# Performance work log

Hardware: AMD Instinct MI355X
Metric: run time of the kernel (lower is better)

## Reference

```python
import jax, jax.numpy as jnp
import numpy as np

B, T, D, DFF = 8, 2048, 1024, 4096
EPS = 1e-6
PLIF_ALPHA = 2.0


@jax.custom_vjp
def spike_fn(m):
    # hard threshold forward, atan surrogate backward (PLIF neuron)
    return (m > 0.0).astype(m.dtype)

def _spk_fwd(m):
    return (m > 0.0).astype(m.dtype), m

def _spk_bwd(m, g):
    ds = PLIF_ALPHA / (2.0 * (1.0 + (jnp.pi * 0.5 * PLIF_ALPHA * m) ** 2))
    return (g * ds,)

spike_fn.defvjp(_spk_fwd, _spk_bwd)


def _rmsnorm(x, w):
    rstd = jax.lax.rsqrt(jnp.mean(x * x, axis=-1, keepdims=True) + EPS)
    return x * rstd * w


def setup_inputs() -> dict:
    key = jax.random.key(0)
    ks = jax.random.split(key, 9)
    sc = 0.02
    return {
        'x': jax.random.normal(ks[0], (B, T, D), jnp.float32),
        'rms_w1': jnp.ones((D,), jnp.float32),
        'rms_w2': jnp.ones((D,), jnp.float32),
        'delta_w': sc * jax.random.normal(ks[1], (D, D), jnp.float32),
        'delta_b': jnp.zeros((D,), jnp.float32),
        'b_w': sc * jax.random.normal(ks[2], (D, D), jnp.float32),
        'b_b': jnp.zeros((D,), jnp.float32),
        'A_log': jnp.log(jnp.linspace(0.5, 2.0, D).astype(jnp.float32)),
        'log_tau': jnp.full((D,), jnp.log(2.0), jnp.float32),
        'plif_thr': jnp.ones((D,), jnp.float32),
        'syn_w': sc * jax.random.normal(ks[3], (D, D), jnp.float32),
        'syn_b': jnp.zeros((D,), jnp.float32),
        'gate_w': sc * jax.random.normal(ks[4], (D, D), jnp.float32),
        'gate_b': jnp.zeros((D,), jnp.float32),
        'ffn_g_w': sc * jax.random.normal(ks[5], (DFF, D), jnp.float32),
        'ffn_u_w': sc * jax.random.normal(ks[6], (DFF, D), jnp.float32),
        'ffn_d_w': sc * jax.random.normal(ks[7], (D, DFF), jnp.float32),
    }


def _forward(x, rms_w1, rms_w2, delta_w, delta_b, b_w, b_b, A_log, log_tau,
             plif_thr, syn_w, syn_b, gate_w, gate_b, ffn_g_w, ffn_u_w, ffn_d_w):
    Bx, Tx, Dx = x.shape
    # --- RMSNorm 1 ---
    y1 = _rmsnorm(x, rms_w1)
    # --- selective-scan style liquid inputs ---
    delta = jax.nn.softplus(jnp.einsum('btd,ed->bte', y1, delta_w) + delta_b)  # [B,T,D]
    bvec = delta * (jnp.einsum('btd,ed->bte', y1, b_w) + b_b)                  # [B,T,D]
    A = jnp.exp(-delta * jnp.exp(A_log))                                        # [B,T,D]

    # --- liquid recurrent scan: h_t = tanh(A_t * h_{t-1} + b_t) ---
    def liquid_step(h, ab):
        a_t, b_t = ab
        h = jnp.tanh(a_t * h + b_t)
        return h, h

    h0 = jnp.zeros((Bx, Dx), x.dtype)
    _, h_post = jax.lax.scan(liquid_step, h0,
                             (jnp.swapaxes(A, 0, 1), jnp.swapaxes(bvec, 0, 1)))
    h_post = jnp.swapaxes(h_post, 0, 1)  # [B,T,D]

    # --- PLIF spiking scan with soft reset ---
    pdec = jnp.exp(-1.0 / jnp.exp(log_tau))  # [D]

    def plif_step(v, h_t):
        v_pre = pdec * v + (1.0 - pdec) * h_t
        s = spike_fn(v_pre - plif_thr)
        return v_pre - s * plif_thr, s

    v0 = jnp.zeros((Bx, Dx), x.dtype)
    _, spike = jax.lax.scan(plif_step, v0, jnp.swapaxes(h_post, 0, 1))
    spike = jnp.swapaxes(spike, 0, 1)

    # --- SEW shortcut + synaptic gate ---
    spike_in = spike + h_post
    syn = jnp.einsum('btd,ed->bte', spike_in, syn_w) + syn_b
    gate = jax.nn.sigmoid(jnp.einsum('btd,ed->bte', spike_in, gate_w) + gate_b)
    x1 = x + syn * gate

    # --- RMSNorm 2 + SwiGLU FFN + residual ---
    y2 = _rmsnorm(x1, rms_w2)
    ffn_act = jax.nn.silu(y2 @ ffn_g_w.T) * (y2 @ ffn_u_w.T)
    return x1 + ffn_act @ ffn_d_w.T


def reference(x, rms_w1, rms_w2, delta_w, delta_b, b_w, b_b, A_log, log_tau,
              plif_thr, syn_w, syn_b, gate_w, gate_b, ffn_g_w, ffn_u_w, ffn_d_w):
    return _forward(x, rms_w1, rms_w2, delta_w, delta_b, b_w, b_b, A_log,
                    log_tau, plif_thr, syn_w, syn_b, gate_w, gate_b,
                    ffn_g_w, ffn_u_w, ffn_d_w)
```

## Files before the change

### kernel.cpp

```cpp
#include <hip/hip_runtime.h>
#include <stdint.h>

#define B_   8
#define T_   2048
#define D_   1024
#define DFF_ 4096
#define M_   (B_ * T_)

typedef __bf16 bf16;
typedef bf16  bf16x8 __attribute__((ext_vector_type(8)));
typedef bf16  bf16x4 __attribute__((ext_vector_type(4)));
typedef float f32x4  __attribute__((ext_vector_type(4)));

#define CAST_LDS(p) ((__attribute__((address_space(3))) void*)(p))
#define CAST_GLB(p) ((const __attribute__((address_space(1))) void*)(p))

struct CvtArgs {
    const float* s[7];
    bf16* d[7];
    int nblk[7];
};

__global__ __launch_bounds__(256) void f2bf_all_kernel(CvtArgs a) {
    int blk = blockIdx.x;
    int seg = 0;
#pragma unroll
    for (int i = 0; i < 7; ++i) seg += (blk >= a.nblk[i]) ? 1 : 0;
    const int base = (seg == 0) ? 0 : a.nblk[seg - 1];
    const int i = ((blk - base) * 256 + threadIdx.x) * 4;
    const float4 v = *(const float4*)(a.s[seg] + i);
    bf16x4 o;
    o[0] = (bf16)v.x; o[1] = (bf16)v.y; o[2] = (bf16)v.z; o[3] = (bf16)v.w;
    *(bf16x4*)(a.d[seg] + i) = o;
}

__global__ __launch_bounds__(256) void rmsnorm_kernel(const float* __restrict__ x,
                                                      const float* __restrict__ w,
                                                      bf16* __restrict__ y) {
    const size_t row = blockIdx.x;
    const int t = threadIdx.x;
    const float4 v = ((const float4*)(x + row * D_))[t];
    float ss = v.x * v.x + v.y * v.y + v.z * v.z + v.w * v.w;
#pragma unroll
    for (int off = 32; off; off >>= 1) ss += __shfl_down(ss, off);
    __shared__ float red[4];
    if ((t & 63) == 0) red[t >> 6] = ss;
    __syncthreads();
    const float total = red[0] + red[1] + red[2] + red[3];
    const float rstd = rsqrtf(total * (1.0f / (float)D_) + 1e-6f);
    const float4 wv = ((const float4*)w)[t];
    bf16x4 o;
    o[0] = (bf16)(v.x * rstd * wv.x);
    o[1] = (bf16)(v.y * rstd * wv.y);
    o[2] = (bf16)(v.z * rstd * wv.z);
    o[3] = (bf16)(v.w * rstd * wv.w);
    ((bf16x4*)(y + row * D_))[t] = o;
}

__global__ __launch_bounds__(256) void rmsnorm_bf_kernel(const bf16* __restrict__ x,
                                                         const float* __restrict__ w,
                                                         bf16* __restrict__ y) {
    const size_t row = blockIdx.x;
    const int t = threadIdx.x;
    const bf16x4 xv = ((const bf16x4*)(x + row * D_))[t];
    float f0 = (float)xv[0], f1 = (float)xv[1], f2 = (float)xv[2], f3 = (float)xv[3];
    float ss = f0 * f0 + f1 * f1 + f2 * f2 + f3 * f3;
#pragma unroll
    for (int off = 32; off; off >>= 1) ss += __shfl_down(ss, off);
    __shared__ float red[4];
    if ((t & 63) == 0) red[t >> 6] = ss;
    __syncthreads();
    const float total = red[0] + red[1] + red[2] + red[3];
    const float rstd = rsqrtf(total * (1.0f / (float)D_) + 1e-6f);
    const float4 wv = ((const float4*)w)[t];
    bf16x4 o;
    o[0] = (bf16)(f0 * rstd * wv.x);
    o[1] = (bf16)(f1 * rstd * wv.y);
    o[2] = (bf16)(f2 * rstd * wv.z);
    o[3] = (bf16)(f3 * rstd * wv.w);
    ((bf16x4*)(y + row * D_))[t] = o;
}

#define SCAN_C  32
#define SCAN_L  (T_ / SCAN_C)
#define SCAN_W  32
#define SCAN_PF 8

template <int N, int W0>
__device__ __forceinline__ void scan_body(const uint32_t* __restrict__ p,
                                          bf16* __restrict__ o, const int ts,
                                          const float pdec, const float om,
                                          const float th) {
    uint32_t buf[SCAN_PF];
#pragma unroll
    for (int i = 0; i < SCAN_PF; ++i) buf[i] = p[(size_t)i * D_];
    float h = 0.0f, v = 0.0f;
#pragma unroll 8
    for (int k = 0; k < N; ++k) {
        const uint32_t w = buf[k & (SCAN_PF - 1)];
        if (k + SCAN_PF < N) buf[k & (SCAN_PF - 1)] = p[(size_t)(k + SCAN_PF) * D_];
        const float a  = __builtin_bit_cast(float, w << 16);
        const float bb = __builtin_bit_cast(float, w & 0xffff0000u);
        const float xv = fmaf(a, h, bb);
        const float e2 = __expf(2.0f * xv);
        h = 1.0f - __fdividef(2.0f, 1.0f + e2);
        const float vpre = fmaf(pdec, v, om * h);
        const float s = (vpre > th) ? 1.0f : 0.0f;
        v = vpre - s * th;
        if (k >= W0) o[(size_t)(ts + k) * D_] = (bf16)(s + h);
    }
}

__global__ __launch_bounds__(256) void scan_kernel(const uint32_t* __restrict__ ABp,
                                                   const float* __restrict__ log_tau,
                                                   const float* __restrict__ thr,
                                                   bf16* __restrict__ sp) {
    const int g = blockIdx.x * 256 + threadIdx.x;
    const int d = g & (D_ - 1);
    const int bc = g >> 10;
    const int b = bc / SCAN_C;
    const int c = bc % SCAN_C;
    const float pdec = __expf(-__expf(-log_tau[d]));
    const float om = 1.0f - pdec;
    const float th = thr[d];
    const int t0 = c * SCAN_L;
    const uint32_t* base = ABp + (size_t)b * (T_ * D_) + d;
    bf16* o = sp + (size_t)b * (T_ * D_) + d;
    if (c == 0) {
        scan_body<SCAN_L, 0>(base, o, 0, pdec, om, th);
    } else {
        const int ts = t0 - SCAN_W;
        scan_body<SCAN_L + SCAN_W, SCAN_W>(base + (size_t)ts * D_, o, ts, pdec, om, th);
    }
}

template <int NB, int MODE>
__global__ __launch_bounds__(256, 2) void gemm_kernel(
    const bf16* __restrict__ A, const bf16* __restrict__ W1, const bf16* __restrict__ W2,
    const int M, const int N, const int K,
    const float* __restrict__ b1, const float* __restrict__ b2,
    const float* __restrict__ extra, const bf16* __restrict__ extra_bf,
    void* __restrict__ outp) {
    __shared__ bf16 As[2][128 * 32];
    __shared__ bf16 Bs[NB][2][128 * 32];

    const int tid = threadIdx.x;
    const int wave = tid >> 6;
    const int lane = tid & 63;
    const int lane15 = lane & 15;
    const int quad = lane >> 4;
    const int m0 = blockIdx.y * 128;
    const int n0 = blockIdx.x * 128;
    const int wm = (wave >> 1) * 64;
    const int wn = (wave & 1) * 64;

    f32x4 acc[NB][4][4] = {};

    const int srow = lane >> 2;
    const int scol = (lane & 3) * 8;
    const bf16* gA = A + (size_t)(m0 + wave * 32 + srow) * K + scol;
    const bf16* gW[2];
    gW[0] = W1 + (size_t)(n0 + wave * 32 + srow) * K + scol;
    if (NB > 1) gW[1] = W2 + (size_t)(n0 + wave * 32 + srow) * K + scol;

    const int lofs = (wave * 32) * 32;

    for (int k0 = 0; k0 < K; k0 += 64) {
#pragma unroll
        for (int h = 0; h < 2; ++h) {
            const int kh = k0 + h * 32;
            bf16* lA = &As[h][lofs];
            __builtin_amdgcn_global_load_lds(CAST_GLB(gA + kh),          CAST_LDS(lA),           16, 0, 0);
            __builtin_amdgcn_global_load_lds(CAST_GLB(gA + kh + 16 * K), CAST_LDS(lA + 16 * 32), 16, 0, 0);
#pragma unroll
            for (int nb = 0; nb < NB; ++nb) {
                bf16* lB = &Bs[nb][h][lofs];
                __builtin_amdgcn_global_load_lds(CAST_GLB(gW[nb] + kh),          CAST_LDS(lB),           16, 0, 0);
                __builtin_amdgcn_global_load_lds(CAST_GLB(gW[nb] + kh + 16 * K), CAST_LDS(lB + 16 * 32), 16, 0, 0);
            }
        }
        __syncthreads();

#pragma unroll
        for (int h = 0; h < 2; ++h) {
            bf16x8 af[4];
#pragma unroll
            for (int i = 0; i < 4; ++i)
                af[i] = *(const bf16x8*)(&As[h][(wm + i * 16 + lane15) * 32 + quad * 8]);
#pragma unroll
            for (int nb = 0; nb < NB; ++nb) {
#pragma unroll
                for (int j = 0; j < 4; ++j) {
                    const bf16x8 bfj = *(const bf16x8*)(&Bs[nb][h][(wn + j * 16 + lane15) * 32 + quad * 8]);
#pragma unroll
                    for (int i = 0; i < 4; ++i)
                        acc[nb][i][j] = __builtin_amdgcn_mfma_f32_16x16x32_bf16(af[i], bfj, acc[nb][i][j], 0, 0, 0);
                }
            }
        }
        __syncthreads();
    }

#pragma unroll
    for (int i = 0; i < 4; ++i) {
#pragma unroll
        for (int r = 0; r < 4; ++r) {
            const int m = m0 + wm + i * 16 + quad * 4 + r;
#pragma unroll
            for (int j = 0; j < 4; ++j) {
                const int n = n0 + wn + j * 16 + lane15;
                const size_t idx = (size_t)m * N + n;
                const float v1 = acc[0][i][j][r];
                if constexpr (MODE == 0) {
                    const float v2 = acc[1][i][j][r];
                    const float dl = v1 + b1[n];
                    const float spv = (dl > 20.0f) ? dl : log1pf(__expf(dl));
                    const float bv = spv * (v2 + b2[n]);
                    const float av = __expf(-spv * __expf(extra[n]));
                    const uint32_t pa = (uint32_t)__builtin_bit_cast(unsigned short, (bf16)av);
                    const uint32_t pb = (uint32_t)__builtin_bit_cast(unsigned short, (bf16)bv);
                    ((uint32_t*)outp)[idx] = pa | (pb << 16);
                } else if constexpr (MODE == 1) {
                    const float v2 = acc[1][i][j][r];
                    const float syn = v1 + b1[n];
                    const float z = v2 + b2[n];
                    const float gate = 1.0f / (1.0f + __expf(-z));
                    ((bf16*)outp)[idx] = (bf16)(extra[idx] + syn * gate);
                } else if constexpr (MODE == 2) {
                    const float v2 = acc[1][i][j][r];
                    const float sg = v1 / (1.0f + __expf(-v1));
                    ((bf16*)outp)[idx] = (bf16)(sg * v2);
                } else {
                    ((float*)outp)[idx] = (float)extra_bf[idx] + v1;
                }
            }
        }
    }
}

extern "C" void kernel_launch(void* const* d_in, const int* in_sizes, int n_in,
                              void* d_out, int out_size, void* d_ws, size_t ws_size,
                              hipStream_t stream) {
    const float* x        = (const float*)d_in[0];
    const float* rms_w1   = (const float*)d_in[1];
    const float* rms_w2   = (const float*)d_in[2];
    const float* delta_w  = (const float*)d_in[3];
    const float* delta_b  = (const float*)d_in[4];
    const float* b_w      = (const float*)d_in[5];
    const float* b_b      = (const float*)d_in[6];
    const float* A_log    = (const float*)d_in[7];
    const float* log_tau  = (const float*)d_in[8];
    const float* plif_thr = (const float*)d_in[9];
    const float* syn_w    = (const float*)d_in[10];
    const float* syn_b    = (const float*)d_in[11];
    const float* gate_w   = (const float*)d_in[12];
    const float* gate_b   = (const float*)d_in[13];
    const float* ffn_g_w  = (const float*)d_in[14];
    const float* ffn_u_w  = (const float*)d_in[15];
    const float* ffn_d_w  = (const float*)d_in[16];

    char* ws = (char*)d_ws;
    const size_t MB = 1024ull * 1024ull;
    bf16* wdelta = (bf16*)(ws + 0 * MB);
    bf16* wb     = (bf16*)(ws + 2 * MB);
    bf16* wsyn   = (bf16*)(ws + 4 * MB);
    bf16* wgate  = (bf16*)(ws + 6 * MB);
    bf16* wg     = (bf16*)(ws + 8 * MB);
    bf16* wu     = (bf16*)(ws + 16 * MB);
    bf16* wd     = (bf16*)(ws + 24 * MB);
    bf16*     y1      = (bf16*)(ws + 32 * MB);
    uint32_t* ABp     = (uint32_t*)(ws + 64 * MB);
    bf16*     spikein = (bf16*)(ws + 128 * MB);
    bf16* x1 = (bf16*)(ws + 160 * MB);
    bf16* y2 = (bf16*)(ws + 224 * MB);
    bf16* act = (bf16*)(ws + 32 * MB);
    float* outF = (float*)d_out;

    const int DD = D_ * D_;
    const int DF = DFF_ * D_;
    const int BD = DD / 1024;
    const int BF = DF / 1024;

    CvtArgs ca;
    ca.s[0] = delta_w; ca.d[0] = wdelta;
    ca.s[1] = b_w;     ca.d[1] = wb;
    ca.s[2] = syn_w;   ca.d[2] = wsyn;
    ca.s[3] = gate_w;  ca.d[3] = wgate;
    ca.s[4] = ffn_g_w; ca.d[4] = wg;
    ca.s[5] = ffn_u_w; ca.d[5] = wu;
    ca.s[6] = ffn_d_w; ca.d[6] = wd;
    int acc_blk = 0;
    const int segblk[7] = {BD, BD, BD, BD, BF, BF, BF};
    for (int i = 0; i < 7; ++i) { acc_blk += segblk[i]; ca.nblk[i] = acc_blk; }
    f2bf_all_kernel<<<acc_blk, 256, 0, stream>>>(ca);

    rmsnorm_kernel<<<M_, 256, 0, stream>>>(x, rms_w1, y1);

    gemm_kernel<2, 0><<<dim3(D_ / 128, M_ / 128), 256, 0, stream>>>(
        y1, wdelta, wb, M_, D_, D_, delta_b, b_b, A_log, nullptr, ABp);

    scan_kernel<<<(B_ * SCAN_C * D_) / 256, 256, 0, stream>>>(ABp, log_tau, plif_thr, spikein);

    gemm_kernel<2, 1><<<dim3(D_ / 128, M_ / 128), 256, 0, stream>>>(
        spikein, wsyn, wgate, M_, D_, D_, syn_b, gate_b, x, nullptr, x1);

    rmsnorm_bf_kernel<<<M_, 256, 0, stream>>>(x1, rms_w2, y2);

    gemm_kernel<2, 2><<<dim3(DFF_ / 128, M_ / 128), 256, 0, stream>>>(
        y2, wg, wu, M_, DFF_, D_, nullptr, nullptr, nullptr, nullptr, act);

    gemm_kernel<1, 3><<<dim3(D_ / 128, M_ / 128), 256, 0, stream>>>(
        act, wd, nullptr, M_, D_, DFF_, nullptr, nullptr, nullptr, x1, outF);
}
```

Baseline: 940.2 us.

## Replace GEMMs with 256x256 8-wave pipelined kernel over interleaved concatenated weights

```diff
diff --git a/kernel.cpp b/kernel.cpp
--- a/kernel.cpp
+++ b/kernel.cpp
@@ -15,23 +15,36 @@
 #define CAST_LDS(p) ((__attribute__((address_space(3))) void*)(p))
 #define CAST_GLB(p) ((const __attribute__((address_space(1))) void*)(p))
 
-struct CvtArgs {
-    const float* s[7];
-    bf16* d[7];
-    int nblk[7];
+struct CatArgs {
+    const float* w1[3];
+    const float* w2[3];
+    bf16* dst[3];
+    int end[3];
 };
 
-__global__ __launch_bounds__(256) void f2bf_all_kernel(CvtArgs a) {
-    int blk = blockIdx.x;
-    int seg = 0;
-#pragma unroll
-    for (int i = 0; i < 7; ++i) seg += (blk >= a.nblk[i]) ? 1 : 0;
-    const int base = (seg == 0) ? 0 : a.nblk[seg - 1];
-    const int i = ((blk - base) * 256 + threadIdx.x) * 4;
-    const float4 v = *(const float4*)(a.s[seg] + i);
+__global__ __launch_bounds__(256) void cvt_cat_kernel(CatArgs a) {
+    const int b = blockIdx.x;
+    const int seg = (b >= a.end[0] ? 1 : 0) + (b >= a.end[1] ? 1 : 0);
+    const int d = b - (seg ? a.end[seg - 1] : 0);
+    const int nt = d >> 8;
+    const int r = d & 255;
+    const float* src = ((r < 128) ? a.w1[seg] : a.w2[seg]) +
+                       (size_t)((nt << 7) + (r & 127)) * D_;
+    bf16* dst = a.dst[seg] + (size_t)d * D_;
+    const int t = threadIdx.x;
+    const float4 v = ((const float4*)src)[t];
     bf16x4 o;
     o[0] = (bf16)v.x; o[1] = (bf16)v.y; o[2] = (bf16)v.z; o[3] = (bf16)v.w;
-    *(bf16x4*)(a.d[seg] + i) = o;
+    ((bf16x4*)dst)[t] = o;
+}
+
+__global__ __launch_bounds__(256) void cvt_plain_kernel(const float* __restrict__ s,
+                                                        bf16* __restrict__ d) {
+    const int i = (blockIdx.x * 256 + threadIdx.x) * 4;
+    const float4 v = *(const float4*)(s + i);
+    bf16x4 o;
+    o[0] = (bf16)v.x; o[1] = (bf16)v.y; o[2] = (bf16)v.z; o[3] = (bf16)v.w;
+    *(bf16x4*)(d + i) = o;
 }
 
 __global__ __launch_bounds__(256) void rmsnorm_kernel(const float* __restrict__ x,
@@ -134,109 +147,201 @@
     }
 }
 
-template <int NB, int MODE>
-__global__ __launch_bounds__(256, 2) void gemm_kernel(
-    const bf16* __restrict__ A, const bf16* __restrict__ W1, const bf16* __restrict__ W2,
-    const int M, const int N, const int K,
+
+#define STG_A(tt, kh)                                                                  \
+  { bf16* l_ = lA0 + ((((tt) & 1) << 1) + (kh)) * 8192;                                \
+    const bf16* g_ = gA + (tt) * 64 + ((kh) << 5);                                     \
+    __builtin_amdgcn_global_load_lds(CAST_GLB(g_), CAST_LDS(l_), 16, 0, 0);            \
+    __builtin_amdgcn_global_load_lds(CAST_GLB(g_ + g2), CAST_LDS(l_ + 4096), 16, 0, 0); }
+#define STG_B(tt, kh)                                                                  \
+  { bf16* l_ = lB0 + ((((tt) & 1) << 1) + (kh)) * 8192;                                \
+    const bf16* g_ = gB + (tt) * 64 + ((kh) << 5);                                     \
+    __builtin_amdgcn_global_load_lds(CAST_GLB(g_), CAST_LDS(l_), 16, 0, 0);            \
+    __builtin_amdgcn_global_load_lds(CAST_GLB(g_ + g2), CAST_LDS(l_ + 4096), 16, 0, 0); }
+#define DSREAD_A(KS, MH)                                                               \
+  { const bf16* As_ = smA + (cb + (KS)) * 8192;                                        \
+    _Pragma("unroll")                                                                  \
+    for (int i = 0; i < 4; ++i) {                                                      \
+      const int row_ = mr128 + (MH) * 64 + i * 16 + lane15;                            \
+      af[i] = *(const bf16x8*)(As_ + row_ * 32 + ((quad ^ ((row_ >> 1) & 3)) << 3));   \
+    } }
+#define DSREAD_B(KS)                                                                   \
+  { const bf16* Bs_ = smB + (cb + (KS)) * 8192;                                        \
+    _Pragma("unroll")                                                                  \
+    for (int j = 0; j < 4; ++j) {                                                      \
+      const int row_ = nc64 + j * 16 + lane15;                                         \
+      bfr[j] = *(const bf16x8*)(Bs_ + row_ * 32 + ((quad ^ ((row_ >> 1) & 3)) << 3));  \
+    } }
+#define MFMA16(MH)                                                                     \
+  __builtin_amdgcn_s_setprio(1);                                                       \
+  _Pragma("unroll")                                                                    \
+  for (int i = 0; i < 4; ++i)                                                          \
+    _Pragma("unroll")                                                                  \
+    for (int j = 0; j < 4; ++j)                                                        \
+      acc[(MH) * 4 + i][j] = __builtin_amdgcn_mfma_f32_16x16x32_bf16(                  \
+          af[i], bfr[j], acc[(MH) * 4 + i][j], 0, 0, 0);                               \
+  __builtin_amdgcn_s_setprio(0);
+#define GBAR() __builtin_amdgcn_s_barrier()
+#define LGKM0() asm volatile("s_waitcnt lgkmcnt(0)" ::: "memory")
+
+template <int MODE>
+__global__ __launch_bounds__(512, 2) void gemm8_kernel(
+    const bf16* __restrict__ A, const bf16* __restrict__ Bw,
+    const int Ncat, const int K, const int Nlog,
     const float* __restrict__ b1, const float* __restrict__ b2,
     const float* __restrict__ extra, const bf16* __restrict__ extra_bf,
     void* __restrict__ outp) {
-    __shared__ bf16 As[2][128 * 32];
-    __shared__ bf16 Bs[NB][2][128 * 32];
+    constexpr bool DUAL = (MODE != 3);
+    __shared__ bf16 smem[65536] __attribute__((aligned(16)));
+    bf16* const smA = smem;
+    bf16* const smB = smem + 32768;
 
     const int tid = threadIdx.x;
     const int wave = tid >> 6;
     const int lane = tid & 63;
     const int lane15 = lane & 15;
     const int quad = lane >> 4;
-    const int m0 = blockIdx.y * 128;
-    const int n0 = blockIdx.x * 128;
-    const int wm = (wave >> 1) * 64;
-    const int wn = (wave & 1) * 64;
-
-    f32x4 acc[NB][4][4] = {};
-
-    const int srow = lane >> 2;
-    const int scol = (lane & 3) * 8;
-    const bf16* gA = A + (size_t)(m0 + wave * 32 + srow) * K + scol;
-    const bf16* gW[2];
-    gW[0] = W1 + (size_t)(n0 + wave * 32 + srow) * K + scol;
-    if (NB > 1) gW[1] = W2 + (size_t)(n0 + wave * 32 + srow) * K + scol;
-
-    const int lofs = (wave * 32) * 32;
-
-    for (int k0 = 0; k0 < K; k0 += 64) {
-#pragma unroll
-        for (int h = 0; h < 2; ++h) {
-            const int kh = k0 + h * 32;
-            bf16* lA = &As[h][lofs];
-            __builtin_amdgcn_global_load_lds(CAST_GLB(gA + kh),          CAST_LDS(lA),           16, 0, 0);
-            __builtin_amdgcn_global_load_lds(CAST_GLB(gA + kh + 16 * K), CAST_LDS(lA + 16 * 32), 16, 0, 0);
-#pragma unroll
-            for (int nb = 0; nb < NB; ++nb) {
-                bf16* lB = &Bs[nb][h][lofs];
-                __builtin_amdgcn_global_load_lds(CAST_GLB(gW[nb] + kh),          CAST_LDS(lB),           16, 0, 0);
-                __builtin_amdgcn_global_load_lds(CAST_GLB(gW[nb] + kh + 16 * K), CAST_LDS(lB + 16 * 32), 16, 0, 0);
-            }
+    const int mr = wave >> 2;
+    const int nc = wave & 3;
+    const int mr128 = mr * 128;
+    const int nc64 = nc * 64;
+
+    int bid = blockIdx.x;
+    const int cpx = gridDim.x >> 3;
+    bid = (bid & 7) * cpx + (bid >> 3);
+    const int NTN = Ncat >> 8;
+    const int nt = bid % NTN;
+    const int mt = bid / NTN;
+
+    const int srow = tid >> 2;
+    const int scol = (((tid & 3) ^ ((srow >> 1) & 3)) << 3);
+    const bf16* const gA = A + (size_t)(mt * 256 + srow) * K + scol;
+    const bf16* const gB = Bw + (size_t)(nt * 256 + srow) * K + scol;
+    const size_t g2 = (size_t)128 * K;
+    bf16* const lA0 = smA + (wave << 9);
+    bf16* const lB0 = smB + (wave << 9);
+
+    const int NT = K >> 6;
+
+    f32x4 acc[8][4] = {};
+    bf16x8 af[4];
+    bf16x8 bfr[4];
+
+    STG_B(0, 0); STG_A(0, 0); STG_B(0, 1); STG_A(0, 1);
+    asm volatile("s_waitcnt vmcnt(4)" ::: "memory");
+    STG_B(1, 0); STG_A(1, 0); STG_B(1, 1);
+    asm volatile("s_waitcnt vmcnt(6)" ::: "memory");
+    GBAR();
+
+    for (int t = 0; t < NT; ++t) {
+        const int cb = (t & 1) << 1;
+
+        DSREAD_A(0, 0); DSREAD_B(0);
+        if (t + 1 < NT) STG_A(t + 1, 1);
+        GBAR(); LGKM0();
+        MFMA16(0);
+        GBAR();
+
+        DSREAD_A(0, 1);
+        if (t + 2 < NT) STG_B(t + 2, 0);
+        GBAR(); LGKM0();
+        MFMA16(1);
+        GBAR();
+
+        DSREAD_A(1, 0); DSREAD_B(1);
+        if (t + 2 < NT) STG_A(t + 2, 0);
+        GBAR(); LGKM0();
+        MFMA16(0);
+        GBAR();
+
+        DSREAD_A(1, 1);
+        if (t + 2 < NT) {
+            STG_B(t + 2, 1);
+            asm volatile("s_waitcnt vmcnt(6)" ::: "memory");
+        } else {
+            asm volatile("s_waitcnt vmcnt(0)" ::: "memory");
+        }
+        GBAR(); LGKM0();
+        MFMA16(1);
+        GBAR();
+    }
+
+    if constexpr (DUAL) {
+        float* const xch = (float*)smem;
+        if (nc >= 2) {
+            float* const dst = xch + (mr * 2 + (nc - 2)) * 8192;
+#pragma unroll
+            for (int i8 = 0; i8 < 8; ++i8)
+#pragma unroll
+                for (int j = 0; j < 4; ++j)
+#pragma unroll
+                    for (int r = 0; r < 4; ++r)
+                        dst[(i8 * 16 + quad * 4 + r) * 64 + j * 16 + lane15] =
+                            acc[i8][j][r];
         }
         __syncthreads();
-
-#pragma unroll
-        for (int h = 0; h < 2; ++h) {
-            bf16x8 af[4];
-#pragma unroll
-            for (int i = 0; i < 4; ++i)
-                af[i] = *(const bf16x8*)(&As[h][(wm + i * 16 + lane15) * 32 + quad * 8]);
-#pragma unroll
-            for (int nb = 0; nb < NB; ++nb) {
-#pragma unroll
-                for (int j = 0; j < 4; ++j) {
-                    const bf16x8 bfj = *(const bf16x8*)(&Bs[nb][h][(wn + j * 16 + lane15) * 32 + quad * 8]);
-#pragma unroll
-                    for (int i = 0; i < 4; ++i)
-                        acc[nb][i][j] = __builtin_amdgcn_mfma_f32_16x16x32_bf16(af[i], bfj, acc[nb][i][j], 0, 0, 0);
+        if (nc < 2) {
+            const float* const src = xch + (mr * 2 + nc) * 8192;
+            const int mbase = mt * 256 + mr128;
+            const int nbase = nt * 128 + nc64;
+#pragma unroll
+            for (int i8 = 0; i8 < 8; ++i8)
+#pragma unroll
+                for (int j = 0; j < 4; ++j)
+#pragma unroll
+                    for (int r = 0; r < 4; ++r) {
+                        const int rl = i8 * 16 + quad * 4 + r;
+                        const int cl = j * 16 + lane15;
+                        const int m = mbase + rl;
+                        const int n = nbase + cl;
+                        const size_t idx = (size_t)m * Nlog + n;
+                        const float v1 = acc[i8][j][r];
+                        const float v2 = src[rl * 64 + cl];
+                        if constexpr (MODE == 0) {
+                            const float dl = v1 + b1[n];
+                            const float spv = (dl > 20.0f) ? dl : log1pf(__expf(dl));
+                            const float bv = spv * (v2 + b2[n]);
+                            const float av = __expf(-spv * __expf(extra[n]));
+                            const uint32_t pa =
+                                (uint32_t)__builtin_bit_cast(unsigned short, (bf16)av);
+                            const uint32_t pb =
+                                (uint32_t)__builtin_bit_cast(unsigned short, (bf16)bv);
+                            ((uint32_t*)outp)[idx] = pa | (pb << 16);
+                        } else if constexpr (MODE == 1) {
+                            const float syn = v1 + b1[n];
+                            const float z = v2 + b2[n];
+                            const float gate = 1.0f / (1.0f + __expf(-z));
+                            ((bf16*)outp)[idx] = (bf16)(extra[idx] + syn * gate);
+                        } else {
+                            const float sg = v1 / (1.0f + __expf(-v1));
+                            ((bf16*)outp)[idx] = (bf16)(sg * v2);
+                        }
+                    }
+        }
+    } else {
+        const int mbase = mt * 256 + mr128;
+        const int nbase = nt * 256 + nc64;
+#pragma unroll
+        for (int i8 = 0; i8 < 8; ++i8)
+#pragma unroll
+            for (int j = 0; j < 4; ++j)
+#pragma unroll
+                for (int r = 0; r < 4; ++r) {
+                    const int m = mbase + i8 * 16 + quad * 4 + r;
+                    const int n = nbase + j * 16 + lane15;
+                    const size_t idx = (size_t)m * Nlog + n;
+                    ((float*)outp)[idx] = (float)extra_bf[idx] + acc[i8][j][r];
                 }
-            }
-        }
-        __syncthreads();
     }
-
-#pragma unroll
-    for (int i = 0; i < 4; ++i) {
-#pragma unroll
-        for (int r = 0; r < 4; ++r) {
-            const int m = m0 + wm + i * 16 + quad * 4 + r;
-#pragma unroll
-            for (int j = 0; j < 4; ++j) {
-                const int n = n0 + wn + j * 16 + lane15;
-                const size_t idx = (size_t)m * N + n;
-                const float v1 = acc[0][i][j][r];
-                if constexpr (MODE == 0) {
-                    const float v2 = acc[1][i][j][r];
-                    const float dl = v1 + b1[n];
-                    const float spv = (dl > 20.0f) ? dl : log1pf(__expf(dl));
-                    const float bv = spv * (v2 + b2[n]);
-                    const float av = __expf(-spv * __expf(extra[n]));
-                    const uint32_t pa = (uint32_t)__builtin_bit_cast(unsigned short, (bf16)av);
-                    const uint32_t pb = (uint32_t)__builtin_bit_cast(unsigned short, (bf16)bv);
-                    ((uint32_t*)outp)[idx] = pa | (pb << 16);
-                } else if constexpr (MODE == 1) {
-                    const float v2 = acc[1][i][j][r];
-                    const float syn = v1 + b1[n];
-                    const float z = v2 + b2[n];
-                    const float gate = 1.0f / (1.0f + __expf(-z));
-                    ((bf16*)outp)[idx] = (bf16)(extra[idx] + syn * gate);
-                } else if constexpr (MODE == 2) {
-                    const float v2 = acc[1][i][j][r];
-                    const float sg = v1 / (1.0f + __expf(-v1));
-                    ((bf16*)outp)[idx] = (bf16)(sg * v2);
-                } else {
-                    ((float*)outp)[idx] = (float)extra_bf[idx] + v1;
-                }
-            }
-        }
-    }
-}
+}
+
+#undef STG_A
+#undef STG_B
+#undef DSREAD_A
+#undef DSREAD_B
+#undef MFMA16
+#undef GBAR
+#undef LGKM0
 
 extern "C" void kernel_launch(void* const* d_in, const int* in_sizes, int n_in,
                               void* d_out, int out_size, void* d_ws, size_t ws_size,
@@ -261,13 +366,10 @@
 
     char* ws = (char*)d_ws;
     const size_t MB = 1024ull * 1024ull;
-    bf16* wdelta = (bf16*)(ws + 0 * MB);
-    bf16* wb     = (bf16*)(ws + 2 * MB);
-    bf16* wsyn   = (bf16*)(ws + 4 * MB);
-    bf16* wgate  = (bf16*)(ws + 6 * MB);
-    bf16* wg     = (bf16*)(ws + 8 * MB);
-    bf16* wu     = (bf16*)(ws + 16 * MB);
-    bf16* wd     = (bf16*)(ws + 24 * MB);
+    bf16* wcat_db = (bf16*)(ws + 0 * MB);
+    bf16* wcat_sg = (bf16*)(ws + 4 * MB);
+    bf16* wcat_gu = (bf16*)(ws + 8 * MB);
+    bf16* wd      = (bf16*)(ws + 24 * MB);
     bf16*     y1      = (bf16*)(ws + 32 * MB);
     uint32_t* ABp     = (uint32_t*)(ws + 64 * MB);
     bf16*     spikein = (bf16*)(ws + 128 * MB);
@@ -276,39 +378,29 @@
     bf16* act = (bf16*)(ws + 32 * MB);
     float* outF = (float*)d_out;
 
-    const int DD = D_ * D_;
-    const int DF = DFF_ * D_;
-    const int BD = DD / 1024;
-    const int BF = DF / 1024;
-
-    CvtArgs ca;
-    ca.s[0] = delta_w; ca.d[0] = wdelta;
-    ca.s[1] = b_w;     ca.d[1] = wb;
-    ca.s[2] = syn_w;   ca.d[2] = wsyn;
-    ca.s[3] = gate_w;  ca.d[3] = wgate;
-    ca.s[4] = ffn_g_w; ca.d[4] = wg;
-    ca.s[5] = ffn_u_w; ca.d[5] = wu;
-    ca.s[6] = ffn_d_w; ca.d[6] = wd;
-    int acc_blk = 0;
-    const int segblk[7] = {BD, BD, BD, BD, BF, BF, BF};
-    for (int i = 0; i < 7; ++i) { acc_blk += segblk[i]; ca.nblk[i] = acc_blk; }
-    f2bf_all_kernel<<<acc_blk, 256, 0, stream>>>(ca);
+    CatArgs ca;
+    ca.w1[0] = delta_w; ca.w2[0] = b_w;     ca.dst[0] = wcat_db;
+    ca.w1[1] = syn_w;   ca.w2[1] = gate_w;  ca.dst[1] = wcat_sg;
+    ca.w1[2] = ffn_g_w; ca.w2[2] = ffn_u_w; ca.dst[2] = wcat_gu;
+    ca.end[0] = 2048; ca.end[1] = 4096; ca.end[2] = 12288;
+    cvt_cat_kernel<<<12288, 256, 0, stream>>>(ca);
+    cvt_plain_kernel<<<(D_ * DFF_) / 1024, 256, 0, stream>>>(ffn_d_w, wd);
 
     rmsnorm_kernel<<<M_, 256, 0, stream>>>(x, rms_w1, y1);
 
-    gemm_kernel<2, 0><<<dim3(D_ / 128, M_ / 128), 256, 0, stream>>>(
-        y1, wdelta, wb, M_, D_, D_, delta_b, b_b, A_log, nullptr, ABp);
+    gemm8_kernel<0><<<(2048 / 256) * (M_ / 256), 512, 0, stream>>>(
+        y1, wcat_db, 2048, D_, D_, delta_b, b_b, A_log, nullptr, ABp);
 
     scan_kernel<<<(B_ * SCAN_C * D_) / 256, 256, 0, stream>>>(ABp, log_tau, plif_thr, spikein);
 
-    gemm_kernel<2, 1><<<dim3(D_ / 128, M_ / 128), 256, 0, stream>>>(
-        spikein, wsyn, wgate, M_, D_, D_, syn_b, gate_b, x, nullptr, x1);
+    gemm8_kernel<1><<<(2048 / 256) * (M_ / 256), 512, 0, stream>>>(
+        spikein, wcat_sg, 2048, D_, D_, syn_b, gate_b, x, nullptr, x1);
 
     rmsnorm_bf_kernel<<<M_, 256, 0, stream>>>(x1, rms_w2, y2);
 
-    gemm_kernel<2, 2><<<dim3(DFF_ / 128, M_ / 128), 256, 0, stream>>>(
-        y2, wg, wu, M_, DFF_, D_, nullptr, nullptr, nullptr, nullptr, act);
-
-    gemm_kernel<1, 3><<<dim3(D_ / 128, M_ / 128), 256, 0, stream>>>(
-        act, wd, nullptr, M_, D_, DFF_, nullptr, nullptr, nullptr, x1, outF);
-}
+    gemm8_kernel<2><<<(8192 / 256) * (M_ / 256), 512, 0, stream>>>(
+        y2, wcat_gu, 8192, D_, DFF_, nullptr, nullptr, nullptr, nullptr, act);
+
+    gemm8_kernel<3><<<(1024 / 256) * (M_ / 256), 512, 0, stream>>>(
+        act, wd, 1024, DFF_, D_, nullptr, nullptr, nullptr, x1, outF);
+}
```

Measured after the change: 1.001 ms. +6.4%, slower.

## Replace down-projection GEMM with 256x256-tile, 8-wave pipelined kernel

Applied to the files above, without the earlier changes.

```diff
diff --git a/kernel.cpp b/kernel.cpp
--- a/kernel.cpp
+++ b/kernel.cpp
@@ -226,17 +226,153 @@
                     const float z = v2 + b2[n];
                     const float gate = 1.0f / (1.0f + __expf(-z));
                     ((bf16*)outp)[idx] = (bf16)(extra[idx] + syn * gate);
-                } else if constexpr (MODE == 2) {
+                } else {
                     const float v2 = acc[1][i][j][r];
                     const float sg = v1 / (1.0f + __expf(-v1));
                     ((bf16*)outp)[idx] = (bf16)(sg * v2);
-                } else {
-                    ((float*)outp)[idx] = (float)extra_bf[idx] + v1;
                 }
             }
         }
     }
 }
+
+
+#define STG_A(tt, kh)                                                                  \
+  { bf16* l_ = lA0 + ((((tt) & 1) << 1) + (kh)) * 8192;                                \
+    const bf16* g_ = gA + (tt) * 64 + ((kh) << 5);                                     \
+    __builtin_amdgcn_global_load_lds(CAST_GLB(g_), CAST_LDS(l_), 16, 0, 0);            \
+    __builtin_amdgcn_global_load_lds(CAST_GLB(g_ + g2), CAST_LDS(l_ + 4096), 16, 0, 0); }
+#define STG_B(tt, kh)                                                                  \
+  { bf16* l_ = lB0 + ((((tt) & 1) << 1) + (kh)) * 8192;                                \
+    const bf16* g_ = gB + (tt) * 64 + ((kh) << 5);                                     \
+    __builtin_amdgcn_global_load_lds(CAST_GLB(g_), CAST_LDS(l_), 16, 0, 0);            \
+    __builtin_amdgcn_global_load_lds(CAST_GLB(g_ + g2), CAST_LDS(l_ + 4096), 16, 0, 0); }
+#define DSREAD_A(KS, MH)                                                               \
+  { const bf16* As_ = smA + (cb + (KS)) * 8192 + swz;                                  \
+    _Pragma("unroll")                                                                  \
+    for (int i = 0; i < 4; ++i)                                                        \
+      af[i] = *(const bf16x8*)(As_ + (mr128 + (MH) * 64 + i * 16 + lane15) * 32);      \
+  }
+#define DSREAD_B(KS)                                                                   \
+  { const bf16* Bs_ = smB + (cb + (KS)) * 8192 + swz;                                  \
+    _Pragma("unroll")                                                                  \
+    for (int j = 0; j < 4; ++j)                                                        \
+      bfr[j] = *(const bf16x8*)(Bs_ + (nc64 + j * 16 + lane15) * 32);                  \
+  }
+#define MFMA16(MH)                                                                     \
+  __builtin_amdgcn_s_setprio(1);                                                       \
+  _Pragma("unroll")                                                                    \
+  for (int i = 0; i < 4; ++i)                                                          \
+    _Pragma("unroll")                                                                  \
+    for (int j = 0; j < 4; ++j)                                                        \
+      acc[(MH) * 4 + i][j] = __builtin_amdgcn_mfma_f32_16x16x32_bf16(                  \
+          af[i], bfr[j], acc[(MH) * 4 + i][j], 0, 0, 0);                               \
+  __builtin_amdgcn_s_setprio(0);
+#define GBAR() __builtin_amdgcn_s_barrier()
+#define LGKM0() asm volatile("s_waitcnt lgkmcnt(0)" ::: "memory")
+
+template <int MODE>
+__global__ __launch_bounds__(512, 2) void gemm8_kernel(
+    const bf16* __restrict__ A, const bf16* __restrict__ Bw,
+    const int Ncat, const int K, const int Nlog,
+    const float* __restrict__ b1, const float* __restrict__ b2,
+    const float* __restrict__ extra, const bf16* __restrict__ extra_bf,
+    void* __restrict__ outp) {
+    __shared__ bf16 smem[65536] __attribute__((aligned(16)));
+    bf16* const smA = smem;
+    bf16* const smB = smem + 32768;
+
+    const int tid = threadIdx.x;
+    const int wave = tid >> 6;
+    const int lane = tid & 63;
+    const int lane15 = lane & 15;
+    const int quad = lane >> 4;
+    const int mr = wave >> 2;
+    const int nc = wave & 3;
+    const int mr128 = mr * 128;
+    const int nc64 = nc * 64;
+    const int swz = (quad ^ ((lane15 >> 1) & 3)) << 3;
+
+    const int xcd = blockIdx.x & 7;
+    const int c = blockIdx.x >> 3;
+    const int mt = xcd * 8 + (c & 7);
+    const int nt = (c >> 5) * 4 + ((c >> 3) & 3);
+
+    const int srow = tid >> 2;
+    const int scol = (((tid & 3) ^ ((srow >> 1) & 3)) << 3);
+    const bf16* const gA = A + (size_t)(mt * 256 + srow) * K + scol;
+    const bf16* const gB = Bw + (size_t)(nt * 256 + srow) * K + scol;
+    const size_t g2 = (size_t)128 * K;
+    bf16* const lA0 = smA + (wave << 9);
+    bf16* const lB0 = smB + (wave << 9);
+
+    const int NT = K >> 6;
+
+    f32x4 acc[8][4] = {};
+    bf16x8 af[4];
+    bf16x8 bfr[4];
+
+    STG_B(0, 0); STG_A(0, 0); STG_B(0, 1); STG_A(0, 1);
+    asm volatile("s_waitcnt vmcnt(4)" ::: "memory");
+    STG_B(1, 0); STG_A(1, 0); STG_B(1, 1);
+    asm volatile("s_waitcnt vmcnt(6)" ::: "memory");
+    GBAR();
+
+    for (int t = 0; t < NT; ++t) {
+        const int cb = (t & 1) << 1;
+
+        DSREAD_A(0, 0); DSREAD_B(0);
+        if (t + 1 < NT) STG_A(t + 1, 1);
+        GBAR(); LGKM0();
+        MFMA16(0);
+        GBAR();
+
+        DSREAD_A(0, 1);
+        if (t + 2 < NT) STG_B(t + 2, 0);
+        GBAR(); LGKM0();
+        MFMA16(1);
+        GBAR();
+
+        DSREAD_A(1, 0); DSREAD_B(1);
+        if (t + 2 < NT) STG_A(t + 2, 0);
+        GBAR(); LGKM0();
+        MFMA16(0);
+        GBAR();
+
+        DSREAD_A(1, 1);
+        if (t + 2 < NT) {
+            STG_B(t + 2, 1);
+            asm volatile("s_waitcnt vmcnt(6)" ::: "memory");
+        } else {
+            asm volatile("s_waitcnt vmcnt(0)" ::: "memory");
+        }
+        GBAR(); LGKM0();
+        MFMA16(1);
+        GBAR();
+    }
+
+    const int mbase = mt * 256 + mr128;
+    const int nbase = nt * 256 + nc64;
+#pragma unroll
+    for (int i8 = 0; i8 < 8; ++i8)
+#pragma unroll
+        for (int j = 0; j < 4; ++j)
+#pragma unroll
+            for (int r = 0; r < 4; ++r) {
+                const int m = mbase + i8 * 16 + quad * 4 + r;
+                const int n = nbase + j * 16 + lane15;
+                const size_t idx = (size_t)m * Nlog + n;
+                ((float*)outp)[idx] = (float)extra_bf[idx] + acc[i8][j][r];
+            }
+}
+
+#undef STG_A
+#undef STG_B
+#undef DSREAD_A
+#undef DSREAD_B
+#undef MFMA16
+#undef GBAR
+#undef LGKM0
 
 extern "C" void kernel_launch(void* const* d_in, const int* in_sizes, int n_in,
                               void* d_out, int out_size, void* d_ws, size_t ws_size,
@@ -309,6 +445,6 @@
     gemm_kernel<2, 2><<<dim3(DFF_ / 128, M_ / 128), 256, 0, stream>>>(
         y2, wg, wu, M_, DFF_, D_, nullptr, nullptr, nullptr, nullptr, act);
 
-    gemm_kernel<1, 3><<<dim3(D_ / 128, M_ / 128), 256, 0, stream>>>(
-        act, wd, nullptr, M_, D_, DFF_, nullptr, nullptr, nullptr, x1, outF);
-}
+    gemm8_kernel<3><<<(1024 / 256) * (M_ / 256), 512, 0, stream>>>(
+        act, wd, 1024, DFF_, D_, nullptr, nullptr, nullptr, x1, outF);
+}
```

Result: faster. 886.4 us (-5.7%).
